# Kernel optimization log

Hardware: AMD Instinct MI355X
Metric: run time of the kernel (lower is better)

The kernel has to match this reference:

```python
import jax, jax.numpy as jnp
import numpy as np

B, T, D_IN, H, K = 8, 1024, 1024, 1024, 3
PAD = (K - 1) // 2


def conv_gates(x, w, b):
    # x: [B,T,C], w: [3H, C, K], b: [3H] -> f,o,z each [B,T,H]
    y = jax.lax.conv_general_dilated(
        x.transpose(0, 2, 1), w, window_strides=(1,), padding=[(PAD, PAD)],
        dimension_numbers=('NCH', 'OIH', 'NCH'))
    g = y.transpose(0, 2, 1) + b  # [B,T,3H]
    f, o, z = jnp.split(g, 3, axis=-1)
    return jax.nn.sigmoid(f), jax.nn.sigmoid(o), jnp.tanh(z)


def fo_pool(f, z):
    # linear recurrence c_t = f_t*c_{t-1} + (1-f_t)*z_t, c_0 = 0; f,z: [B,T,H]
    def step(c, fz):
        ft, zt = fz
        c = ft * c + (1.0 - ft) * zt
        return c, c
    init = jnp.zeros((f.shape[0], f.shape[2]), f.dtype)
    _, cells = jax.lax.scan(step, init, (f.transpose(1, 0, 2), z.transpose(1, 0, 2)))
    return cells.transpose(1, 0, 2)  # [B,T,H]


def qrnn_layer(x, wf, bf, wr, br):
    # forward direction
    f, o, z = conv_gates(x, wf, bf)
    cells = fo_pool(f, z)
    h = cells * o
    # reverse direction: scan from the end (flip, scan, flip back)
    fr, orv, zr = conv_gates(x, wr, br)
    rcells = jnp.flip(fo_pool(jnp.flip(fr, 1), jnp.flip(zr, 1)), 1)
    rh = rcells * orv
    out = jnp.concatenate([h, rh], -1)                      # [B,T,2H]
    last_h = jnp.concatenate([h[:, -1], rh[:, -1]], -1)     # [B,2H]
    last_c = jnp.concatenate([cells[:, -1], rcells[:, -1]], -1)
    return out, last_h, last_c


def setup_inputs() -> dict:
    key = jax.random.key(0)
    ks = jax.random.split(key, 9)
    x = jax.random.normal(ks[0], (B, T, D_IN), jnp.float32)
    lengths = jnp.full((B,), T, dtype=jnp.int64)
    s = 0.02
    # layer 0: in=D_IN, layer 1: in=2H (bidirectional concat)
    w0f = jax.random.normal(ks[1], (3 * H, D_IN, K), jnp.float32) * s
    b0f = jnp.zeros((3 * H,), jnp.float32)
    w0r = jax.random.normal(ks[2], (3 * H, D_IN, K), jnp.float32) * s
    b0r = jnp.zeros((3 * H,), jnp.float32)
    w1f = jax.random.normal(ks[3], (3 * H, 2 * H, K), jnp.float32) * s
    b1f = jnp.zeros((3 * H,), jnp.float32)
    w1r = jax.random.normal(ks[4], (3 * H, 2 * H, K), jnp.float32) * s
    b1r = jnp.zeros((3 * H,), jnp.float32)
    return {"x": x, "lengths": lengths, "w0f": w0f, "b0f": b0f, "w0r": w0r,
            "b0r": b0r, "w1f": w1f, "b1f": b1f, "w1r": w1r, "b1r": b1r}


def reference(x, lengths, w0f, b0f, w0r, b0r, w1f, b1f, w1r, b1r):
    out0, h0, c0 = qrnn_layer(x, w0f, b0f, w0r, b0r)
    out1, h1, c1 = qrnn_layer(out0, w1f, b1f, w1r, b1r)
    # torch: cat along dim 0 then view(num_dir*num_layers, B, H)
    hidden = jnp.concatenate([h0, h1], 0).reshape(4, x.shape[0], H)
    cell = jnp.concatenate([c0, c1], 0).reshape(4, x.shape[0], H)
    return out1, hidden, cell
```

## Files before the change

### kernel.cpp

```cpp
#include <hip/hip_runtime.h>
#include <math.h>

#define BB 8
#define TT 1024
#define HDIM 1024
#define G3 3072
#define NCH 32
#define TC 32

#define SW(r) (((r) >> 1) & 3)

typedef __attribute__((ext_vector_type(8))) short bf16x8;
typedef __attribute__((ext_vector_type(4))) float f32x4;

__device__ __forceinline__ unsigned short f2bf(float f) {
  union { float f; unsigned int u; } c; c.f = f;
  unsigned int u = c.u;
  return (unsigned short)((u + 0x7FFFu + ((u >> 16) & 1u)) >> 16);
}

__device__ __forceinline__ void load_lds16(const void* g, void* l) {
  __builtin_amdgcn_global_load_lds(
      (const __attribute__((address_space(1))) void*)g,
      (__attribute__((address_space(3))) void*)l, 16, 0, 0);
}

__global__ __launch_bounds__(256) void cvt_x_kernel(const float* __restrict__ in,
                                                    unsigned short* __restrict__ out, int n) {
  int i = (blockIdx.x * 256 + threadIdx.x) * 4;
  if (i >= n) return;
  float4 v = *(const float4*)(in + i);
  ushort4 o;
  o.x = f2bf(v.x); o.y = f2bf(v.y); o.z = f2bf(v.z); o.w = f2bf(v.w);
  *(ushort4*)(out + i) = o;
}

template<int C>
__global__ __launch_bounds__(256) void cvt_w_kernel(const float* __restrict__ in,
                                                    unsigned short* __restrict__ out) {
  int o = blockIdx.x * 256 + threadIdx.x;
  int c = o & (C - 1);
  int jk = o / C;
  int j = jk % G3;
  int k = jk / G3;
  out[o] = f2bf(in[(size_t)j * (3 * C) + (size_t)c * 3 + k]);
}

template<int C>
__global__ __launch_bounds__(256) void conv_mfma_kernel(
    const unsigned short* __restrict__ x,
    const unsigned short* __restrict__ wt,
    const float* __restrict__ bias,
    float* __restrict__ g)
{
  const int L    = blockIdx.x;
  const int xcd  = L & 7;
  const int sL   = L >> 3;
  const int jt   = xcd * 3 + (sL % 3);
  const int rest = sL / 3;
  const int t0 = (rest & 7) * 128;
  const int j0 = jt * 128;
  const int b  = rest >> 3;

  const int tid  = threadIdx.x;
  const int lane = tid & 63;
  const int wave = tid >> 6;
  const int wm = wave >> 1, wn = wave & 1;

  __shared__ unsigned short As[130 * 32];
  __shared__ unsigned short Bs[3 * 128 * 32];

  f32x4 acc[4][4];
  #pragma unroll
  for (int i = 0; i < 4; i++)
    #pragma unroll
    for (int u = 0; u < 4; u++) acc[i][u] = (f32x4){0.f, 0.f, 0.f, 0.f};

  const unsigned short* xb = x + (size_t)b * TT * C;
  const int srow  = lane >> 2;
  const int sslot = lane & 3;
  const int rq = lane >> 4;
  const int rl = lane & 15;

  for (int c0 = 0; c0 < C; c0 += 32) {
    __syncthreads();
    #pragma unroll
    for (int cc = 0; cc < 2; ++cc) {
      int lrow0 = 1 + wave * 32 + cc * 16;
      int lrow  = lrow0 + srow;
      int t = t0 + lrow - 1;
      int q = sslot ^ SW(lrow);
      load_lds16(xb + (size_t)t * C + c0 + q * 8, &As[lrow0 * 32]);
    }
    #pragma unroll
    for (int cc = 0; cc < 6; ++cc) {
      int R0 = (wave * 6 + cc) * 16;
      int R  = R0 + srow;
      int k = R >> 7;
      int j = R & 127;
      int q = sslot ^ SW(R);
      load_lds16(wt + (size_t)k * (G3 * C) + (size_t)(j0 + j) * C + c0 + q * 8,
                 &Bs[R0 * 32]);
    }
    if (tid < 8) {
      int lr = (tid < 4) ? 0 : 129;
      int s  = tid & 3;
      int t  = t0 + lr - 1;
      int q  = s ^ SW(lr);
      uint4 v = make_uint4(0, 0, 0, 0);
      if (t >= 0 && t < TT) v = *(const uint4*)(xb + (size_t)t * C + c0 + q * 8);
      *(uint4*)&As[lr * 32 + s * 8] = v;
    }
    __syncthreads();

    #pragma unroll
    for (int k = 0; k < 3; ++k) {
      bf16x8 af[4], bfr[4];
      #pragma unroll
      for (int im = 0; im < 4; ++im) {
        int lrow = wm * 64 + im * 16 + rl + k;
        af[im] = *(const bf16x8*)&As[lrow * 32 + ((rq ^ SW(lrow)) * 8)];
      }
      #pragma unroll
      for (int in = 0; in < 4; ++in) {
        int R = k * 128 + wn * 64 + in * 16 + rl;
        bfr[in] = *(const bf16x8*)&Bs[R * 32 + ((rq ^ SW(R)) * 8)];
      }
      #pragma unroll
      for (int im = 0; im < 4; ++im)
        #pragma unroll
        for (int in = 0; in < 4; ++in)
          acc[im][in] = __builtin_amdgcn_mfma_f32_16x16x32_bf16(
              af[im], bfr[in], acc[im][in], 0, 0, 0);
    }
  }

  const bool is_tanh = (j0 >= 2 * HDIM);
  const int row_in_tile = (lane >> 4) * 4;
  float* gb = g + (size_t)b * TT * G3;
  #pragma unroll
  for (int in = 0; in < 4; ++in) {
    int j = j0 + wn * 64 + in * 16 + rl;
    float bv = bias[j];
    #pragma unroll
    for (int im = 0; im < 4; ++im) {
      int tl = wm * 64 + im * 16 + row_in_tile;
      #pragma unroll
      for (int r = 0; r < 4; ++r) {
        float s = acc[im][in][r] + bv;
        float v;
        if (is_tanh) v = 1.f - 2.f / (__expf(2.f * s) + 1.f);
        else         v = 1.f / (1.f + __expf(-s));
        gb[(size_t)(t0 + tl + r) * G3 + j] = v;
      }
    }
  }
}

__global__ __launch_bounds__(256) void pool_chunk_kernel(
    const float* __restrict__ g, float* __restrict__ a_arr,
    float* __restrict__ b_arr, int dir)
{
  int idx = blockIdx.x * 256 + threadIdx.x;
  int h  = idx & (HDIM - 1);
  int b  = (idx >> 10) & (BB - 1);
  int ch = idx >> 13;
  const float* gb = g + (size_t)b * TT * G3 + h;
  float a = 1.f, bacc = 0.f;
  #pragma unroll 8
  for (int s = ch * TC; s < ch * TC + TC; ++s) {
    int t = dir ? (TT - 1 - s) : s;
    size_t go = (size_t)t * G3;
    float f = gb[go];
    float z = gb[go + 2 * HDIM];
    bacc = f * bacc + (1.f - f) * z;
    a *= f;
  }
  a_arr[idx] = a;
  b_arr[idx] = bacc;
}

__global__ __launch_bounds__(256) void pool_scan_kernel(
    const float* __restrict__ a_arr, const float* __restrict__ b_arr,
    float* __restrict__ cinit)
{
  int bh = blockIdx.x * 256 + threadIdx.x;
  float c = 0.f;
  #pragma unroll
  for (int ch = 0; ch < NCH; ++ch) {
    cinit[ch * (BB * HDIM) + bh] = c;
    c = a_arr[ch * (BB * HDIM) + bh] * c + b_arr[ch * (BB * HDIM) + bh];
  }
}

template<int OUT_BF16>
__global__ __launch_bounds__(256) void pool_apply_kernel(
    const float* __restrict__ g, const float* __restrict__ cinit,
    void* __restrict__ out, float* __restrict__ hid, float* __restrict__ cell,
    int dir, int layer)
{
  int idx = blockIdx.x * 256 + threadIdx.x;
  int h  = idx & (HDIM - 1);
  int b  = (idx >> 10) & (BB - 1);
  int ch = idx >> 13;
  const float* gb = g + (size_t)b * TT * G3 + h;
  const int coloff = dir * HDIM;
  float c = cinit[idx];
  #pragma unroll 8
  for (int s = ch * TC; s < ch * TC + TC; ++s) {
    int t = dir ? (TT - 1 - s) : s;
    size_t go = (size_t)t * G3;
    float f = gb[go];
    float o = gb[go + HDIM];
    float z = gb[go + 2 * HDIM];
    c = f * c + (1.f - f) * z;
    float hv = c * o;
    size_t oo = ((size_t)b * TT + t) * (2 * HDIM) + coloff + h;
    if (OUT_BF16) ((unsigned short*)out)[oo] = f2bf(hv);
    else          ((float*)out)[oo] = hv;
    if (t == TT - 1) {
      size_t off = (size_t)layer * (BB * 2 * HDIM) + (size_t)b * (2 * HDIM) + coloff + h;
      hid[off] = hv;
      cell[off] = c;
    }
  }
}

extern "C" void kernel_launch(void* const* d_in, const int* in_sizes, int n_in,
                              void* d_out, int out_size, void* d_ws, size_t ws_size,
                              hipStream_t stream) {
  const float* x   = (const float*)d_in[0];
  const float* w0f = (const float*)d_in[2];
  const float* b0f = (const float*)d_in[3];
  const float* w0r = (const float*)d_in[4];
  const float* b0r = (const float*)d_in[5];
  const float* w1f = (const float*)d_in[6];
  const float* b1f = (const float*)d_in[7];
  const float* w1r = (const float*)d_in[8];
  const float* b1r = (const float*)d_in[9];

  float* out1 = (float*)d_out;
  float* hid  = out1 + (size_t)BB * TT * 2 * HDIM;
  float* cell = hid + 4 * BB * HDIM;

  char* ws = (char*)d_ws;
  size_t off = 0;
  float*          g     = (float*)(ws + off);  off += (size_t)BB * TT * G3 * 4;
  unsigned short* out0b = (unsigned short*)(ws + off); off += (size_t)BB * TT * 2 * HDIM * 2;
  unsigned short* xb16  = (unsigned short*)(ws + off); off += (size_t)BB * TT * 1024 * 2;
  unsigned short* wt    = (unsigned short*)(ws + off); off += (size_t)3 * G3 * 2048 * 2;
  float* a_arr = (float*)(ws + off); off += (size_t)NCH * BB * HDIM * 4;
  float* b_arr = (float*)(ws + off); off += (size_t)NCH * BB * HDIM * 4;
  float* cinit = (float*)(ws + off); off += (size_t)NCH * BB * HDIM * 4;

  dim3 blk(256);
  dim3 cgrd(8 * 24 * 8);
  dim3 chgrd(NCH * BB * HDIM / 256);
  dim3 scgrd(BB * HDIM / 256);

  int nx = BB * TT * 1024;
  cvt_x_kernel<<<nx / (256 * 4), blk, 0, stream>>>(x, xb16, nx);

  #define RUN_POOL(OUTB, outp, dir, layer)                                         \
    pool_chunk_kernel<<<chgrd, blk, 0, stream>>>(g, a_arr, b_arr, dir);            \
    pool_scan_kernel<<<scgrd, blk, 0, stream>>>(a_arr, b_arr, cinit);              \
    pool_apply_kernel<OUTB><<<chgrd, blk, 0, stream>>>(g, cinit, outp, hid, cell,  \
                                                       dir, layer);

  cvt_w_kernel<1024><<<3 * G3 * 1024 / 256, blk, 0, stream>>>(w0f, wt);
  conv_mfma_kernel<1024><<<cgrd, blk, 0, stream>>>(xb16, wt, b0f, g);
  RUN_POOL(1, out0b, 0, 0)

  cvt_w_kernel<1024><<<3 * G3 * 1024 / 256, blk, 0, stream>>>(w0r, wt);
  conv_mfma_kernel<1024><<<cgrd, blk, 0, stream>>>(xb16, wt, b0r, g);
  RUN_POOL(1, out0b, 1, 0)

  cvt_w_kernel<2048><<<3 * G3 * 2048 / 256, blk, 0, stream>>>(w1f, wt);
  conv_mfma_kernel<2048><<<cgrd, blk, 0, stream>>>(out0b, wt, b1f, g);
  RUN_POOL(0, out1, 0, 1)

  cvt_w_kernel<2048><<<3 * G3 * 2048 / 256, blk, 0, stream>>>(w1r, wt);
  conv_mfma_kernel<2048><<<cgrd, blk, 0, stream>>>(out0b, wt, b1r, g);
  RUN_POOL(0, out1, 1, 1)
  #undef RUN_POOL
}
```

Measured before the change: 1.369 ms.

## Double-buffer conv GEMM LDS staging and pre-pad inputs to drop boundary loads

The conv GEMM kernel now double-buffers its A and B LDS tiles, issuing the next chunk's async global-to-LDS loads before computing on the current chunk. It replaces the two __syncthreads per step with explicit vmcnt waits, barriers and priority hints. To make every A row loadable through the async path, the bf16 activations are stored with one zero row of padding at each end of the time axis, which removes the per-step scalar boundary loads. This doubles LDS use per block, which may reduce occupancy, and relies on hand-counted vmcnt values that must match the number of outstanding loads per wave.

```diff
diff --git a/kernel.cpp b/kernel.cpp
--- a/kernel.cpp
+++ b/kernel.cpp
@@ -7,6 +7,7 @@
 #define G3 3072
 #define NCH 32
 #define TC 32
+#define TP (TT + 2)
 
 #define SW(r) (((r) >> 1) & 3)
 
@@ -25,14 +26,26 @@
       (__attribute__((address_space(3))) void*)l, 16, 0, 0);
 }
 
-__global__ __launch_bounds__(256) void cvt_x_kernel(const float* __restrict__ in,
-                                                    unsigned short* __restrict__ out, int n) {
+__global__ __launch_bounds__(256) void cvt_x_pad_kernel(const float* __restrict__ in,
+                                                        unsigned short* __restrict__ out) {
+  int b = blockIdx.y;
   int i = (blockIdx.x * 256 + threadIdx.x) * 4;
-  if (i >= n) return;
-  float4 v = *(const float4*)(in + i);
-  ushort4 o;
-  o.x = f2bf(v.x); o.y = f2bf(v.y); o.z = f2bf(v.z); o.w = f2bf(v.w);
-  *(ushort4*)(out + i) = o;
+  int r = i >> 10;
+  int c = i & 1023;
+  ushort4 o = make_ushort4(0, 0, 0, 0);
+  if (r >= 1 && r <= TT) {
+    float4 v = *(const float4*)(in + ((size_t)b * TT + (r - 1)) * 1024 + c);
+    o.x = f2bf(v.x); o.y = f2bf(v.y); o.z = f2bf(v.z); o.w = f2bf(v.w);
+  }
+  *(ushort4*)(out + (size_t)b * TP * 1024 + i) = o;
+}
+
+__global__ __launch_bounds__(256) void zero_pad_kernel(unsigned short* __restrict__ p) {
+  int i = blockIdx.x * 256 + threadIdx.x;
+  int b = i >> 12;
+  int r = (i >> 11) & 1;
+  int c = i & 2047;
+  p[((size_t)b * TP + (r ? (TT + 1) : 0)) * 2048 + c] = 0;
 }
 
 template<int C>
@@ -67,8 +80,8 @@
   const int wave = tid >> 6;
   const int wm = wave >> 1, wn = wave & 1;
 
-  __shared__ unsigned short As[130 * 32];
-  __shared__ unsigned short Bs[3 * 128 * 32];
+  __shared__ unsigned short As[2][144 * 32];
+  __shared__ unsigned short Bs[2][384 * 32];
 
   f32x4 acc[4][4];
   #pragma unroll
@@ -76,55 +89,73 @@
     #pragma unroll
     for (int u = 0; u < 4; u++) acc[i][u] = (f32x4){0.f, 0.f, 0.f, 0.f};
 
-  const unsigned short* xb = x + (size_t)b * TT * C;
+  const unsigned short* xb = x + (size_t)b * TP * C;
   const int srow  = lane >> 2;
   const int sslot = lane & 3;
   const int rq = lane >> 4;
   const int rl = lane & 15;
 
-  for (int c0 = 0; c0 < C; c0 += 32) {
-    __syncthreads();
+  auto stage = [&](int sel, int c0) {
+    unsigned short* Ab = &As[sel][0];
+    unsigned short* Bb = &Bs[sel][0];
     #pragma unroll
     for (int cc = 0; cc < 2; ++cc) {
-      int lrow0 = 1 + wave * 32 + cc * 16;
+      int call  = wave * 2 + cc;
+      int lrow0 = call << 4;
       int lrow  = lrow0 + srow;
-      int t = t0 + lrow - 1;
       int q = sslot ^ SW(lrow);
-      load_lds16(xb + (size_t)t * C + c0 + q * 8, &As[lrow0 * 32]);
+      load_lds16(xb + (size_t)(t0 + lrow) * C + c0 + q * 8, Ab + lrow0 * 32);
+    }
+    if (wave == 3) {
+      int lrow0 = 128;
+      int lrow  = lrow0 + srow;
+      int q = sslot ^ SW(lrow);
+      load_lds16(xb + (size_t)(t0 + lrow) * C + c0 + q * 8, Ab + lrow0 * 32);
     }
     #pragma unroll
     for (int cc = 0; cc < 6; ++cc) {
-      int R0 = (wave * 6 + cc) * 16;
+      int R0 = (wave * 6 + cc) << 4;
       int R  = R0 + srow;
       int k = R >> 7;
       int j = R & 127;
       int q = sslot ^ SW(R);
       load_lds16(wt + (size_t)k * (G3 * C) + (size_t)(j0 + j) * C + c0 + q * 8,
-                 &Bs[R0 * 32]);
-    }
-    if (tid < 8) {
-      int lr = (tid < 4) ? 0 : 129;
-      int s  = tid & 3;
-      int t  = t0 + lr - 1;
-      int q  = s ^ SW(lr);
-      uint4 v = make_uint4(0, 0, 0, 0);
-      if (t >= 0 && t < TT) v = *(const uint4*)(xb + (size_t)t * C + c0 + q * 8);
-      *(uint4*)&As[lr * 32 + s * 8] = v;
-    }
-    __syncthreads();
-
+                 Bb + R0 * 32);
+    }
+  };
+
+  constexpr int NSTEP = C / 32;
+
+  stage(0, 0);
+
+  #pragma unroll 2
+  for (int it = 0; it < NSTEP; ++it) {
+    const int cur = it & 1;
+    if (it + 1 < NSTEP) {
+      stage(cur ^ 1, (it + 1) * 32);
+      if (wave == 3) asm volatile("s_waitcnt vmcnt(9)" ::: "memory");
+      else           asm volatile("s_waitcnt vmcnt(8)" ::: "memory");
+    } else {
+      asm volatile("s_waitcnt vmcnt(0)" ::: "memory");
+    }
+    __builtin_amdgcn_s_barrier();
+    __builtin_amdgcn_sched_barrier(0);
+
+    const unsigned short* Ac = &As[cur][0];
+    const unsigned short* Bc = &Bs[cur][0];
+    __builtin_amdgcn_s_setprio(1);
     #pragma unroll
     for (int k = 0; k < 3; ++k) {
       bf16x8 af[4], bfr[4];
       #pragma unroll
       for (int im = 0; im < 4; ++im) {
         int lrow = wm * 64 + im * 16 + rl + k;
-        af[im] = *(const bf16x8*)&As[lrow * 32 + ((rq ^ SW(lrow)) * 8)];
+        af[im] = *(const bf16x8*)&Ac[lrow * 32 + ((rq ^ SW(lrow)) * 8)];
       }
       #pragma unroll
       for (int in = 0; in < 4; ++in) {
         int R = k * 128 + wn * 64 + in * 16 + rl;
-        bfr[in] = *(const bf16x8*)&Bs[R * 32 + ((rq ^ SW(R)) * 8)];
+        bfr[in] = *(const bf16x8*)&Bc[R * 32 + ((rq ^ SW(R)) * 8)];
       }
       #pragma unroll
       for (int im = 0; im < 4; ++im)
@@ -133,6 +164,8 @@
           acc[im][in] = __builtin_amdgcn_mfma_f32_16x16x32_bf16(
               af[im], bfr[in], acc[im][in], 0, 0, 0);
     }
+    __builtin_amdgcn_s_setprio(0);
+    __builtin_amdgcn_s_barrier();
   }
 
   const bool is_tanh = (j0 >= 2 * HDIM);
@@ -215,9 +248,13 @@
     float z = gb[go + 2 * HDIM];
     c = f * c + (1.f - f) * z;
     float hv = c * o;
-    size_t oo = ((size_t)b * TT + t) * (2 * HDIM) + coloff + h;
-    if (OUT_BF16) ((unsigned short*)out)[oo] = f2bf(hv);
-    else          ((float*)out)[oo] = hv;
+    if (OUT_BF16) {
+      size_t oo = ((size_t)b * TP + t + 1) * (2 * HDIM) + coloff + h;
+      ((unsigned short*)out)[oo] = f2bf(hv);
+    } else {
+      size_t oo = ((size_t)b * TT + t) * (2 * HDIM) + coloff + h;
+      ((float*)out)[oo] = hv;
+    }
     if (t == TT - 1) {
       size_t off = (size_t)layer * (BB * 2 * HDIM) + (size_t)b * (2 * HDIM) + coloff + h;
       hid[off] = hv;
@@ -246,8 +283,8 @@
   char* ws = (char*)d_ws;
   size_t off = 0;
   float*          g     = (float*)(ws + off);  off += (size_t)BB * TT * G3 * 4;
-  unsigned short* out0b = (unsigned short*)(ws + off); off += (size_t)BB * TT * 2 * HDIM * 2;
-  unsigned short* xb16  = (unsigned short*)(ws + off); off += (size_t)BB * TT * 1024 * 2;
+  unsigned short* out0b = (unsigned short*)(ws + off); off += (size_t)BB * TP * 2 * HDIM * 2;
+  unsigned short* xb16  = (unsigned short*)(ws + off); off += (size_t)BB * TP * 1024 * 2;
   unsigned short* wt    = (unsigned short*)(ws + off); off += (size_t)3 * G3 * 2048 * 2;
   float* a_arr = (float*)(ws + off); off += (size_t)NCH * BB * HDIM * 4;
   float* b_arr = (float*)(ws + off); off += (size_t)NCH * BB * HDIM * 4;
@@ -258,8 +295,8 @@
   dim3 chgrd(NCH * BB * HDIM / 256);
   dim3 scgrd(BB * HDIM / 256);
 
-  int nx = BB * TT * 1024;
-  cvt_x_kernel<<<nx / (256 * 4), blk, 0, stream>>>(x, xb16, nx);
+  cvt_x_pad_kernel<<<dim3(TP, BB), blk, 0, stream>>>(x, xb16);
+  zero_pad_kernel<<<2 * BB * 2048 / 256, blk, 0, stream>>>(out0b);
 
   #define RUN_POOL(OUTB, outp, dir, layer)                                         \
     pool_chunk_kernel<<<chgrd, blk, 0, stream>>>(g, a_arr, b_arr, dir);            \
```

New measurement: 1.354 ms. Within noise of the previous version (-1.1%).
